# Kernel optimization log

Hardware: AMD Instinct MI355X
Metric: run time of the kernel (lower is better)

The kernel has to match this reference:

```python
import jax, jax.numpy as jnp
import numpy as np

N_NODES = 50000
N_EDGES = 1600000
NEG_SLOPE = 0.2


def setup_inputs() -> dict:
    key = jax.random.key(0)
    ks = jax.random.split(key, 11)
    s = 0.1  # small init scale
    return {
        "x": jax.random.normal(ks[0], (N_NODES, 128), dtype=jnp.float32),
        "edge_index": jax.random.randint(ks[1], (2, N_EDGES), 0, N_NODES, dtype=jnp.int64),
        "W1": jax.random.normal(ks[2], (128, 128), dtype=jnp.float32) * s,
        "att_src1": jax.random.normal(ks[3], (2, 64), dtype=jnp.float32) * s,
        "att_dst1": jax.random.normal(ks[4], (2, 64), dtype=jnp.float32) * s,
        "b1": jax.random.normal(ks[5], (128,), dtype=jnp.float32) * s,
        "W2": jax.random.normal(ks[6], (128, 64), dtype=jnp.float32) * s,
        "att_src2": jax.random.normal(ks[7], (1, 64), dtype=jnp.float32) * s,
        "att_dst2": jax.random.normal(ks[8], (1, 64), dtype=jnp.float32) * s,
        "b2": jax.random.normal(ks[9], (64,), dtype=jnp.float32) * s,
    }


def gat_conv(x, W, a_src, a_dst, bias, src, dst, n_nodes):
    # x: [N, F_in]; W: [F_in, H*C]; a_src/a_dst: [H, C]; bias: [H*C]
    H, C = a_src.shape
    xl = (x @ W).reshape(n_nodes, H, C)                 # [N,H,C]
    alpha_s = jnp.einsum('nhc,hc->nh', xl, a_src)       # [N,H]
    alpha_d = jnp.einsum('nhc,hc->nh', xl, a_dst)       # [N,H]
    e = jax.nn.leaky_relu(alpha_s[src] + alpha_d[dst], NEG_SLOPE)  # [E,H]
    # segment softmax over edges sharing the same destination node
    m = jax.ops.segment_max(e, dst, num_segments=n_nodes)          # [N,H]
    m = jnp.where(jnp.isfinite(m), m, 0.0)
    e = jnp.exp(e - m[dst])
    denom = jax.ops.segment_sum(e, dst, num_segments=n_nodes)      # [N,H]
    alpha = e / denom[dst]                               # self-loops guarantee denom > 0
    msg = xl[src] * alpha[:, :, None]                    # [E,H,C]
    out = jax.ops.segment_sum(msg, dst, num_segments=n_nodes)      # [N,H,C]
    return out.reshape(n_nodes, H * C) + bias


def reference(x, edge_index, W1, att_src1, att_dst1, b1, W2, att_src2, att_dst2, b2):
    n = x.shape[0]
    # PyG GATConv default add_self_loops=True
    loops = jnp.arange(n, dtype=edge_index.dtype)
    src = jnp.concatenate([edge_index[0], loops])
    dst = jnp.concatenate([edge_index[1], loops])

    h = gat_conv(x, W1, att_src1, att_dst1, b1, src, dst, n)   # [N, 128]
    h = jax.nn.relu(h)                                          # dropout p=0 (eval)
    h = gat_conv(h, W2, att_src2, att_dst2, b2, src, dst, n)   # [N, 64]
    h = jax.nn.relu(h)
    return h
```

## Files before the change

kernel.cpp:

```cpp
#include <hip/hip_runtime.h>
#include <cstdint>
#include <cstddef>

#define NEG_SLOPE 0.2f

#define NB 128
#define LOG_NB 7
#define MAXK 512

__device__ inline unsigned short f2bf(float f) {
    unsigned int u = __float_as_uint(f);
    u += 0x7FFFu + ((u >> 16) & 1u);
    return (unsigned short)(u >> 16);
}
__device__ inline float bf_lo(unsigned int u) { return __uint_as_float(u << 16); }
__device__ inline float bf_hi(unsigned int u) { return __uint_as_float(u & 0xFFFF0000u); }
__device__ inline float bfu(unsigned short u) { return __uint_as_float((unsigned int)u << 16); }

__global__ __launch_bounds__(256) void sort_count_kernel(const int* __restrict__ ei, int E,
                                                         int K, int CH, int* __restrict__ bcnt) {
    __shared__ int hist[4 * MAXK];
    int tid = threadIdx.x;
    int wiw = tid >> 6;
    for (int i = tid; i < K; i += 256) {
        hist[i] = 0; hist[MAXK + i] = 0; hist[2 * MAXK + i] = 0; hist[3 * MAXK + i] = 0;
    }
    __syncthreads();
    int lo = blockIdx.x * CH;
    int hi = lo + CH; if (hi > E) hi = E;
    for (int e = lo + tid; e < hi; e += 256)
        atomicAdd(&hist[wiw * MAXK + (ei[(size_t)E + e] >> LOG_NB)], 1);
    __syncthreads();
    for (int i = tid; i < K; i += 256) {
        int c = hist[i] + hist[MAXK + i] + hist[2 * MAXK + i] + hist[3 * MAXK + i];
        if (c) atomicAdd(&bcnt[i], c);
    }
}

__global__ void sort_scan_kernel(const int* __restrict__ bcnt, int* __restrict__ boff,
                                 int* __restrict__ bcur, int K, int E) {
    __shared__ int buf[MAXK];
    int tid = threadIdx.x;
    int v = (tid < K) ? bcnt[tid] : 0;
    buf[tid] = v;
    __syncthreads();
    for (int o = 1; o < MAXK; o <<= 1) {
        int t = (tid >= o) ? buf[tid - o] : 0;
        __syncthreads();
        buf[tid] += t;
        __syncthreads();
    }
    if (tid < K) {
        int ex = buf[tid] - v;
        boff[tid] = ex;
        bcur[tid] = ex;
    }
    if (tid == K) boff[K] = E;
}


template <int FOUT, int H, int ROWS, bool BF16IN>
__device__ __forceinline__ void gemm_att_body(const void* __restrict__ Xv,
                                              const float* __restrict__ W,
                                              const float* __restrict__ attS,
                                              const float* __restrict__ attD,
                                              unsigned short* __restrict__ Ybf,
                                              float* __restrict__ as_,
                                              float* __restrict__ ad_, int N, int bid,
                                              float* sX, float* sW) {
    constexpr int CG  = FOUT / 4;
    constexpr int RR  = (ROWS * FOUT) / 1024;
    constexpr int LDX = 36;
    int tid = threadIdx.x;
    int rowbase = bid * ROWS;
    int cg = tid % CG;
    int rg = tid / CG;
    int r0 = rg * RR;

    float acc[RR][4];
#pragma unroll
    for (int i = 0; i < RR; i++)
#pragma unroll
        for (int c = 0; c < 4; c++) acc[i][c] = 0.f;

    for (int k0 = 0; k0 < 128; k0 += 32) {
        __syncthreads();
        for (int idx = tid; idx < ROWS * 8; idx += 256) {
            int r = idx >> 3, q = idx & 7;
            int row = rowbase + r;
            float4 val;
            if (row < N) {
                if constexpr (BF16IN) {
                    const unsigned short* Xb = (const unsigned short*)Xv;
                    ushort4 raw = *(const ushort4*)&Xb[(size_t)row * 128 + k0 + q * 4];
                    val = make_float4(bfu(raw.x), bfu(raw.y), bfu(raw.z), bfu(raw.w));
                } else {
                    const float* X = (const float*)Xv;
                    val = *(const float4*)&X[(size_t)row * 128 + k0 + q * 4];
                }
            } else {
                val = make_float4(0.f, 0.f, 0.f, 0.f);
            }
            *(float4*)&sX[r * LDX + q * 4] = val;
        }
        for (int idx = tid; idx < 8 * FOUT; idx += 256)
            *(float4*)&sW[idx * 4] = *(const float4*)&W[(size_t)k0 * FOUT + idx * 4];
        __syncthreads();
        for (int k = 0; k < 32; k += 4) {
            float4 xr[RR];
#pragma unroll
            for (int i = 0; i < RR; i++)
                xr[i] = *(const float4*)&sX[(r0 + i) * LDX + k];
#pragma unroll
            for (int kk = 0; kk < 4; kk++) {
                float4 wv = ((const float4*)(sW + (size_t)(k + kk) * FOUT))[cg];
#pragma unroll
                for (int i = 0; i < RR; i++) {
                    float xv = (&xr[i].x)[kk];
                    acc[i][0] = fmaf(xv, wv.x, acc[i][0]);
                    acc[i][1] = fmaf(xv, wv.y, acc[i][1]);
                    acc[i][2] = fmaf(xv, wv.z, acc[i][2]);
                    acc[i][3] = fmaf(xv, wv.w, acc[i][3]);
                }
            }
        }
    }

#pragma unroll
    for (int i = 0; i < RR; i++) {
        int row = rowbase + r0 + i;
        if (row < N) {
            ushort4 v;
            v.x = f2bf(acc[i][0]); v.y = f2bf(acc[i][1]);
            v.z = f2bf(acc[i][2]); v.w = f2bf(acc[i][3]);
            *(ushort4*)(Ybf + (size_t)row * FOUT + cg * 4) = v;
        }
    }

    float4 asv = ((const float4*)attS)[cg];
    float4 adv = ((const float4*)attD)[cg];
    int head = (H == 2) ? (cg >> 4) : 0;
#pragma unroll
    for (int i = 0; i < RR; i++) {
        float ps = acc[i][0] * asv.x + acc[i][1] * asv.y + acc[i][2] * asv.z + acc[i][3] * asv.w;
        float pd = acc[i][0] * adv.x + acc[i][1] * adv.y + acc[i][2] * adv.z + acc[i][3] * adv.w;
#pragma unroll
        for (int o = 1; o <= 8; o <<= 1) { ps += __shfl_xor(ps, o); pd += __shfl_xor(pd, o); }
        int row = rowbase + r0 + i;
        if ((tid & 15) == 0 && row < N) {
            as_[(size_t)row * H + head] = ps;
            ad_[(size_t)row * H + head] = pd;
        }
    }
}

__global__ __launch_bounds__(256) void scatter_gemm1_kernel(const int* __restrict__ ei, int E,
                                                            int K, int CH, int* __restrict__ bcur,
                                                            unsigned int* __restrict__ bkt,
                                                            const float* __restrict__ X,
                                                            const float* __restrict__ W1,
                                                            const float* __restrict__ attS,
                                                            const float* __restrict__ attD,
                                                            unsigned short* __restrict__ Ybf,
                                                            float* __restrict__ as_,
                                                            float* __restrict__ ad_, int N, int G) {
    __shared__ float sX[64 * 36];
    __shared__ float sW[32 * 128];
    if (blockIdx.x < G) {
        int* hist = (int*)sX;
        int* base = (int*)sW;
        int* cur2 = (int*)sW + MAXK;
        int tid = threadIdx.x;
        int wiw = tid >> 6;
        for (int i = tid; i < K; i += 256) {
            hist[i] = 0; hist[MAXK + i] = 0; hist[2 * MAXK + i] = 0; hist[3 * MAXK + i] = 0;
        }
        __syncthreads();
        int lo = blockIdx.x * CH;
        int hi = lo + CH; if (hi > E) hi = E;
        for (int e = lo + tid; e < hi; e += 256)
            atomicAdd(&hist[wiw * MAXK + (ei[(size_t)E + e] >> LOG_NB)], 1);
        __syncthreads();
        for (int i = tid; i < K; i += 256) {
            int c = hist[i] + hist[MAXK + i] + hist[2 * MAXK + i] + hist[3 * MAXK + i];
            base[i] = c ? atomicAdd(&bcur[i], c) : 0;
            cur2[i] = 0;
        }
        __syncthreads();
        for (int e = lo + tid; e < hi; e += 256) {
            int s = ei[e];
            int d = ei[(size_t)E + e];
            int k = d >> LOG_NB;
            int r = atomicAdd(&cur2[k], 1);
            bkt[(size_t)base[k] + r] = (unsigned int)s | ((unsigned int)d << 16);
        }
    } else {
        gemm_att_body<128, 2, 64, false>(X, W1, attS, attD, Ybf, as_, ad_, N, blockIdx.x - G, sX, sW);
    }
}

__global__ __launch_bounds__(256) void gemm2_kernel(const unsigned short* __restrict__ X,
                                                    const float* __restrict__ W,
                                                    const float* __restrict__ attS,
                                                    const float* __restrict__ attD,
                                                    unsigned short* __restrict__ Ybf,
                                                    float* __restrict__ as_,
                                                    float* __restrict__ ad_, int N) {
    __shared__ float sX[64 * 36];
    __shared__ float sW[32 * 64];
    gemm_att_body<64, 1, 64, true>(X, W, attS, attD, Ybf, as_, ad_, N, blockIdx.x, sX, sW);
}

__global__ __launch_bounds__(256) void sort_finalize_kernel(const unsigned int* __restrict__ bkt,
                                                            const int* __restrict__ boff,
                                                            int* __restrict__ off,
                                                            unsigned int* __restrict__ csrc, int N) {
    __shared__ int nhist[4 * NB];
    __shared__ int part[256];
    __shared__ int loff[NB];
    int k = blockIdx.x;
    int tid = threadIdx.x;
    int wiw = tid >> 6;
    int node0 = k << LOG_NB;
    int nh = N - node0; if (nh > NB) nh = NB;
    int beg = boff[k], end = boff[k + 1];
    for (int i = tid; i < NB; i += 256) {
        nhist[i] = 0; nhist[NB + i] = 0; nhist[2 * NB + i] = 0; nhist[3 * NB + i] = 0;
    }
    __syncthreads();
    for (int e = beg + tid; e < end; e += 256)
        atomicAdd(&nhist[wiw * NB + ((bkt[e] >> 16) - node0)], 1);
    __syncthreads();
    int i0 = 2 * tid, i1 = 2 * tid + 1;
    int v0 = (i0 < nh) ? nhist[i0] + nhist[NB + i0] + nhist[2 * NB + i0] + nhist[3 * NB + i0] + 1 : 0;
    int v1 = (i1 < nh) ? nhist[i1] + nhist[NB + i1] + nhist[2 * NB + i1] + nhist[3 * NB + i1] + 1 : 0;
    part[tid] = v0 + v1;
    __syncthreads();
    for (int o = 1; o < 256; o <<= 1) {
        int t = (tid >= o) ? part[tid - o] : 0;
        __syncthreads();
        part[tid] += t;
        __syncthreads();
    }
    int gbase = beg + node0;
    int base = gbase + ((tid > 0) ? part[tid - 1] : 0);
    if (i0 < nh) loff[i0] = base;
    if (i1 < nh) loff[i1] = base + v0;
    __syncthreads();
    for (int i = tid; i < nh; i += 256) {
        int node = node0 + i;
        off[node] = loff[i];
        csrc[loff[i]] = (unsigned int)node | ((unsigned int)node << 16);
        nhist[i] = loff[i] + 1;
    }
    if (node0 + nh == N && tid == 0) off[N] = gbase + part[255];
    __syncthreads();
    for (int e = beg + tid; e < end; e += 256) {
        unsigned int p = bkt[e];
        int pos = atomicAdd(&nhist[(p >> 16) - node0], 1);
        csrc[pos] = p;
    }
}


__global__ __launch_bounds__(256) void agg1_kernel(const unsigned short* __restrict__ xl,
                                                   const float* __restrict__ as_,
                                                   const float* __restrict__ ad_,
                                                   const float* __restrict__ bias,
                                                   const int* __restrict__ off,
                                                   const unsigned int* __restrict__ csrc,
                                                   unsigned short* __restrict__ out, int N) {
    __shared__ float4 sps[4][64];
    int wiw  = threadIdx.x >> 6;
    int lane = threadIdx.x & 63;
    int node = blockIdx.x * 4 + wiw;
    if (node >= N) return;
    int beg = off[node], end = off[node + 1];
    int deg = end - beg;
    float2 adn = ((const float2*)ad_)[node];

    int cl  = lane & 15;
    int sub = lane >> 4;
    int hd1 = (cl >> 3) & 1;
    float acc[8];
#pragma unroll
    for (int i = 0; i < 8; i++) acc[i] = 0.f;
    const char* xbase = (const char*)xl + cl * 16;

    if (deg <= 64) {
        int so = 0;
        float t0 = -1e30f, t1 = -1e30f;
        if (lane < deg) {
            int s = (int)(csrc[beg + lane] & 0xFFFFu);
            so = s << 8;
            float2 asv = ((const float2*)as_)[s];
            t0 = asv.x + adn.x; t0 = t0 > 0.f ? t0 : NEG_SLOPE * t0;
            t1 = asv.y + adn.y; t1 = t1 > 0.f ? t1 : NEG_SLOPE * t1;
        }
        float m0 = t0, m1 = t1;
#pragma unroll
        for (int o = 32; o; o >>= 1) {
            m0 = fmaxf(m0, __shfl_xor(m0, o));
            m1 = fmaxf(m1, __shfl_xor(m1, o));
        }
        float e0 = (lane < deg) ? __expf(t0 - m0) : 0.f;
        float e1 = (lane < deg) ? __expf(t1 - m1) : 0.f;
        float s0 = e0, s1 = e1;
#pragma unroll
        for (int o = 32; o; o >>= 1) { s0 += __shfl_xor(s0, o); s1 += __shfl_xor(s1, o); }
        sps[wiw][lane] = make_float4(e0 / s0, e1 / s1, __int_as_float(so), 0.f);
        int iters = (deg + 3) >> 2;
#pragma unroll 8
        for (int j = 0; j < iters; j++) {
            float4 q = sps[wiw][j * 4 + sub];
            float a  = hd1 ? q.y : q.x;
            uint4 v  = *(const uint4*)(xbase + __float_as_int(q.z));
            acc[0] = fmaf(a, bf_lo(v.x), acc[0]); acc[1] = fmaf(a, bf_hi(v.x), acc[1]);
            acc[2] = fmaf(a, bf_lo(v.y), acc[2]); acc[3] = fmaf(a, bf_hi(v.y), acc[3]);
            acc[4] = fmaf(a, bf_lo(v.z), acc[4]); acc[5] = fmaf(a, bf_hi(v.z), acc[5]);
            acc[6] = fmaf(a, bf_lo(v.w), acc[6]); acc[7] = fmaf(a, bf_hi(v.w), acc[7]);
        }
    } else {
        float m0 = -1e30f, m1 = -1e30f;
        for (int b = beg; b < end; b += 64) {
            int e = b + lane;
            if (e < end) {
                int s = (int)(csrc[e] & 0xFFFFu);
                float2 asv = ((const float2*)as_)[s];
                float t0 = asv.x + adn.x; t0 = t0 > 0.f ? t0 : NEG_SLOPE * t0;
                float t1 = asv.y + adn.y; t1 = t1 > 0.f ? t1 : NEG_SLOPE * t1;
                m0 = fmaxf(m0, t0); m1 = fmaxf(m1, t1);
            }
        }
#pragma unroll
        for (int o = 32; o; o >>= 1) {
            m0 = fmaxf(m0, __shfl_xor(m0, o));
            m1 = fmaxf(m1, __shfl_xor(m1, o));
        }
        float s0 = 0.f, s1 = 0.f;
        for (int b = beg; b < end; b += 64) {
            int e = b + lane;
            if (e < end) {
                int s = (int)(csrc[e] & 0xFFFFu);
                float2 asv = ((const float2*)as_)[s];
                float t0 = asv.x + adn.x; t0 = t0 > 0.f ? t0 : NEG_SLOPE * t0;
                float t1 = asv.y + adn.y; t1 = t1 > 0.f ? t1 : NEG_SLOPE * t1;
                s0 += __expf(t0 - m0); s1 += __expf(t1 - m1);
            }
        }
#pragma unroll
        for (int o = 32; o; o >>= 1) { s0 += __shfl_xor(s0, o); s1 += __shfl_xor(s1, o); }
        float i0 = 1.f / s0, i1 = 1.f / s1;
        for (int b = beg; b < end; b += 64) {
            int cnt = end - b; if (cnt > 64) cnt = 64;
            float p0 = 0.f, p1 = 0.f; int so = 0;
            if (lane < cnt) {
                int s = (int)(csrc[b + lane] & 0xFFFFu);
                so = s << 8;
                float2 asv = ((const float2*)as_)[s];
                float t0 = asv.x + adn.x; t0 = t0 > 0.f ? t0 : NEG_SLOPE * t0;
                float t1 = asv.y + adn.y; t1 = t1 > 0.f ? t1 : NEG_SLOPE * t1;
                p0 = __expf(t0 - m0) * i0; p1 = __expf(t1 - m1) * i1;
            }
            sps[wiw][lane] = make_float4(p0, p1, __int_as_float(so), 0.f);
            int iters = (cnt + 3) >> 2;
#pragma unroll 8
            for (int j = 0; j < iters; j++) {
                float4 q = sps[wiw][j * 4 + sub];
                float a  = hd1 ? q.y : q.x;
                uint4 v  = *(const uint4*)(xbase + __float_as_int(q.z));
                acc[0] = fmaf(a, bf_lo(v.x), acc[0]); acc[1] = fmaf(a, bf_hi(v.x), acc[1]);
                acc[2] = fmaf(a, bf_lo(v.y), acc[2]); acc[3] = fmaf(a, bf_hi(v.y), acc[3]);
                acc[4] = fmaf(a, bf_lo(v.z), acc[4]); acc[5] = fmaf(a, bf_hi(v.z), acc[5]);
                acc[6] = fmaf(a, bf_lo(v.w), acc[6]); acc[7] = fmaf(a, bf_hi(v.w), acc[7]);
            }
        }
    }
#pragma unroll
    for (int o = 16; o <= 32; o <<= 1)
#pragma unroll
        for (int i = 0; i < 8; i++) acc[i] += __shfl_xor(acc[i], o);
    if (sub == 0) {
        const float* bp = bias + cl * 8;
        unsigned int w0 = (unsigned int)f2bf(fmaxf(acc[0] + bp[0], 0.f)) |
                          ((unsigned int)f2bf(fmaxf(acc[1] + bp[1], 0.f)) << 16);
        unsigned int w1 = (unsigned int)f2bf(fmaxf(acc[2] + bp[2], 0.f)) |
                          ((unsigned int)f2bf(fmaxf(acc[3] + bp[3], 0.f)) << 16);
        unsigned int w2 = (unsigned int)f2bf(fmaxf(acc[4] + bp[4], 0.f)) |
                          ((unsigned int)f2bf(fmaxf(acc[5] + bp[5], 0.f)) << 16);
        unsigned int w3 = (unsigned int)f2bf(fmaxf(acc[6] + bp[6], 0.f)) |
                          ((unsigned int)f2bf(fmaxf(acc[7] + bp[7], 0.f)) << 16);
        uint4 pack = make_uint4(w0, w1, w2, w3);
        *(uint4*)(out + (size_t)node * 128 + cl * 8) = pack;
    }
}


__global__ __launch_bounds__(256) void agg2_kernel(const unsigned short* __restrict__ xl,
                                                   const float* __restrict__ as_,
                                                   const float* __restrict__ ad_,
                                                   const float* __restrict__ bias,
                                                   const int* __restrict__ off,
                                                   const unsigned int* __restrict__ csrc,
                                                   float* __restrict__ out, int N) {
    __shared__ float2 sps[4][64];
    int wiw  = threadIdx.x >> 6;
    int lane = threadIdx.x & 63;
    int node = blockIdx.x * 4 + wiw;
    if (node >= N) return;
    int beg = off[node], end = off[node + 1];
    int deg = end - beg;
    float adn = ad_[node];

    int cl  = lane & 7;
    int sub = lane >> 3;
    float acc[8];
#pragma unroll
    for (int i = 0; i < 8; i++) acc[i] = 0.f;
    const char* xbase = (const char*)xl + cl * 16;

    if (deg <= 64) {
        int so = 0;
        float t = -1e30f;
        if (lane < deg) {
            int s = (int)(csrc[beg + lane] & 0xFFFFu);
            so = s << 7;
            t = as_[s] + adn;
            t = t > 0.f ? t : NEG_SLOPE * t;
        }
        float m = t;
#pragma unroll
        for (int o = 32; o; o >>= 1) m = fmaxf(m, __shfl_xor(m, o));
        float evv = (lane < deg) ? __expf(t - m) : 0.f;
        float sum = evv;
#pragma unroll
        for (int o = 32; o; o >>= 1) sum += __shfl_xor(sum, o);
        sps[wiw][lane] = make_float2(evv / sum, __int_as_float(so));
        int iters = (deg + 7) >> 3;
#pragma unroll 8
        for (int j = 0; j < iters; j++) {
            float2 q = sps[wiw][j * 8 + sub];
            float a  = q.x;
            uint4 v  = *(const uint4*)(xbase + __float_as_int(q.y));
            acc[0] = fmaf(a, bf_lo(v.x), acc[0]); acc[1] = fmaf(a, bf_hi(v.x), acc[1]);
            acc[2] = fmaf(a, bf_lo(v.y), acc[2]); acc[3] = fmaf(a, bf_hi(v.y), acc[3]);
            acc[4] = fmaf(a, bf_lo(v.z), acc[4]); acc[5] = fmaf(a, bf_hi(v.z), acc[5]);
            acc[6] = fmaf(a, bf_lo(v.w), acc[6]); acc[7] = fmaf(a, bf_hi(v.w), acc[7]);
        }
    } else {
        float m = -1e30f;
        for (int b = beg; b < end; b += 64) {
            int e = b + lane;
            if (e < end) {
                float t = as_[csrc[e] & 0xFFFFu] + adn;
                t = t > 0.f ? t : NEG_SLOPE * t;
                m = fmaxf(m, t);
            }
        }
#pragma unroll
        for (int o = 32; o; o >>= 1) m = fmaxf(m, __shfl_xor(m, o));
        float sum = 0.f;
        for (int b = beg; b < end; b += 64) {
            int e = b + lane;
            if (e < end) {
                float t = as_[csrc[e] & 0xFFFFu] + adn;
                t = t > 0.f ? t : NEG_SLOPE * t;
                sum += __expf(t - m);
            }
        }
#pragma unroll
        for (int o = 32; o; o >>= 1) sum += __shfl_xor(sum, o);
        float inv = 1.f / sum;
        for (int b = beg; b < end; b += 64) {
            int cnt = end - b; if (cnt > 64) cnt = 64;
            float p = 0.f; int so = 0;
            if (lane < cnt) {
                int s = (int)(csrc[b + lane] & 0xFFFFu);
                so = s << 7;
                float t = as_[s] + adn;
                t = t > 0.f ? t : NEG_SLOPE * t;
                p = __expf(t - m) * inv;
            }
            sps[wiw][lane] = make_float2(p, __int_as_float(so));
            int iters = (cnt + 7) >> 3;
#pragma unroll 8
            for (int j = 0; j < iters; j++) {
                float2 q = sps[wiw][j * 8 + sub];
                float a  = q.x;
                uint4 v  = *(const uint4*)(xbase + __float_as_int(q.y));
                acc[0] = fmaf(a, bf_lo(v.x), acc[0]); acc[1] = fmaf(a, bf_hi(v.x), acc[1]);
                acc[2] = fmaf(a, bf_lo(v.y), acc[2]); acc[3] = fmaf(a, bf_hi(v.y), acc[3]);
                acc[4] = fmaf(a, bf_lo(v.z), acc[4]); acc[5] = fmaf(a, bf_hi(v.z), acc[5]);
                acc[6] = fmaf(a, bf_lo(v.w), acc[6]); acc[7] = fmaf(a, bf_hi(v.w), acc[7]);
            }
        }
    }
#pragma unroll
    for (int o = 8; o <= 32; o <<= 1)
#pragma unroll
        for (int i = 0; i < 8; i++) acc[i] += __shfl_xor(acc[i], o);
    if (sub == 0) {
        float* op = out + (size_t)node * 64 + cl * 8;
        const float* bp = bias + cl * 8;
#pragma unroll
        for (int i = 0; i < 8; i++) op[i] = fmaxf(acc[i] + bp[i], 0.f);
    }
}


extern "C" void kernel_launch(void* const* d_in, const int* in_sizes, int n_in,
                              void* d_out, int out_size, void* d_ws, size_t ws_size,
                              hipStream_t stream) {
    const float* x        = (const float*)d_in[0];
    const int*   ei       = (const int*)d_in[1];
    const float* W1       = (const float*)d_in[2];
    const float* attS1    = (const float*)d_in[3];
    const float* attD1    = (const float*)d_in[4];
    const float* b1       = (const float*)d_in[5];
    const float* W2       = (const float*)d_in[6];
    const float* attS2    = (const float*)d_in[7];
    const float* attD2    = (const float*)d_in[8];
    const float* b2       = (const float*)d_in[9];
    float* out            = (float*)d_out;

    int N  = in_sizes[0] / 128;
    int E  = in_sizes[1] / 2;
    int EE = E + N;
    int K  = (N + NB - 1) >> LOG_NB;

    char* w = (char*)d_ws;
    auto alloc = [&](size_t bytes) -> void* {
        void* p = (void*)w;
        w += (bytes + 255) & ~(size_t)255;
        return p;
    };
    int*   bcnt = (int*)alloc((size_t)(K + 1) * 4);
    int*   boff = (int*)alloc((size_t)(K + 1) * 4);
    int*   bcur = (int*)alloc((size_t)(K + 1) * 4);
    int*   off  = (int*)alloc((size_t)(N + 1) * 4);
    unsigned int* csrc = (unsigned int*)alloc((size_t)EE * 4);
    unsigned int* bkt  = (unsigned int*)alloc((size_t)E * 4);
    unsigned short* xl1 = (unsigned short*)alloc((size_t)N * 128 * 2);
    float* sd1  = (float*)alloc((size_t)N * 2 * 4);
    float* dd1  = (float*)alloc((size_t)N * 2 * 4);
    unsigned short* h1 = (unsigned short*)alloc((size_t)N * 128 * 2);

    unsigned short* xl2 = xl1;
    float* sd2 = sd1;
    float* dd2 = dd1;

    hipMemsetAsync(bcnt, 0, (size_t)(K + 1) * 4, stream);

    int G   = 256;
    int CH  = (E + G - 1) / G;
    int GB1 = (N + 63) / 64;
    sort_count_kernel<<<G, 256, 0, stream>>>(ei, E, K, CH, bcnt);
    sort_scan_kernel<<<1, MAXK, 0, stream>>>(bcnt, boff, bcur, K, E);
    scatter_gemm1_kernel<<<G + GB1, 256, 0, stream>>>(ei, E, K, CH, bcur, bkt,
                                                      x, W1, attS1, attD1, xl1, sd1, dd1, N, G);
    sort_finalize_kernel<<<K, 256, 0, stream>>>(bkt, boff, off, csrc, N);

    agg1_kernel<<<(N + 3) / 4, 256, 0, stream>>>(xl1, sd1, dd1, b1, off, csrc, h1, N);

    gemm2_kernel<<<(N + 63) / 64, 256, 0, stream>>>(h1, W2, attS2, attD2, xl2, sd2, dd2, N);
    agg2_kernel<<<(N + 3) / 4, 256, 0, stream>>>(xl2, sd2, dd2, b2, off, csrc, out, N);
}
```

Measured before the change: 298.8 us.

## Split layer-1 aggregation into alpha pass and feature-chunked gather over chunked xl layout

Layer-1 GEMM now writes its bf16 output in four column chunks of 32 features (chunk-major, 64 bytes per node per chunk). A separate alpha1 kernel computes the per-edge softmax weights once and stores them as fp16 packed with the source index. A chunked aggregation kernel then gathers one chunk at a time, with blocks for different chunks interleaved. The aim is a smaller per-chunk working set (about 3.2 MB) that stays cache-resident during the random gathers. The cost is an extra kernel launch, an extra write and read of two per-edge arrays, and fp16 precision on the attention weights.

```diff
diff --git a/kernel.cpp b/kernel.cpp
--- a/kernel.cpp
+++ b/kernel.cpp
@@ -1,4 +1,5 @@
 #include <hip/hip_runtime.h>
+#include <hip/hip_fp16.h>
 #include <cstdint>
 #include <cstddef>
 
@@ -16,6 +17,7 @@
 __device__ inline float bf_lo(unsigned int u) { return __uint_as_float(u << 16); }
 __device__ inline float bf_hi(unsigned int u) { return __uint_as_float(u & 0xFFFF0000u); }
 __device__ inline float bfu(unsigned short u) { return __uint_as_float((unsigned int)u << 16); }
+__device__ inline float lrelu(float t) { return t > 0.f ? t : NEG_SLOPE * t; }
 
 __global__ __launch_bounds__(256) void sort_count_kernel(const int* __restrict__ ei, int E,
                                                          int K, int CH, int* __restrict__ bcnt) {
@@ -59,7 +61,7 @@
 }
 
 
-template <int FOUT, int H, int ROWS, bool BF16IN>
+template <int FOUT, int H, int ROWS, bool BF16IN, bool CHUNK_OUT>
 __device__ __forceinline__ void gemm_att_body(const void* __restrict__ Xv,
                                               const float* __restrict__ W,
                                               const float* __restrict__ attS,
@@ -133,7 +135,13 @@
             ushort4 v;
             v.x = f2bf(acc[i][0]); v.y = f2bf(acc[i][1]);
             v.z = f2bf(acc[i][2]); v.w = f2bf(acc[i][3]);
-            *(ushort4*)(Ybf + (size_t)row * FOUT + cg * 4) = v;
+            if constexpr (CHUNK_OUT) {
+                int chunk = cg >> 3;
+                int wc = (cg & 7) * 4;
+                *(ushort4*)(Ybf + ((size_t)chunk * N + row) * 32 + wc) = v;
+            } else {
+                *(ushort4*)(Ybf + (size_t)row * FOUT + cg * 4) = v;
+            }
         }
     }
 
@@ -195,7 +203,8 @@
             bkt[(size_t)base[k] + r] = (unsigned int)s | ((unsigned int)d << 16);
         }
     } else {
-        gemm_att_body<128, 2, 64, false>(X, W1, attS, attD, Ybf, as_, ad_, N, blockIdx.x - G, sX, sW);
+        gemm_att_body<128, 2, 64, false, true>(X, W1, attS, attD, Ybf, as_, ad_, N,
+                                               blockIdx.x - G, sX, sW);
     }
 }
 
@@ -208,7 +217,7 @@
                                                     float* __restrict__ ad_, int N) {
     __shared__ float sX[64 * 36];
     __shared__ float sW[32 * 64];
-    gemm_att_body<64, 1, 64, true>(X, W, attS, attD, Ybf, as_, ad_, N, blockIdx.x, sX, sW);
+    gemm_att_body<64, 1, 64, true, false>(X, W, attS, attD, Ybf, as_, ad_, N, blockIdx.x, sX, sW);
 }
 
 __global__ __launch_bounds__(256) void sort_finalize_kernel(const unsigned int* __restrict__ bkt,
@@ -263,14 +272,12 @@
 }
 
 
-__global__ __launch_bounds__(256) void agg1_kernel(const unsigned short* __restrict__ xl,
-                                                   const float* __restrict__ as_,
-                                                   const float* __restrict__ ad_,
-                                                   const float* __restrict__ bias,
-                                                   const int* __restrict__ off,
-                                                   const unsigned int* __restrict__ csrc,
-                                                   unsigned short* __restrict__ out, int N) {
-    __shared__ float4 sps[4][64];
+__global__ __launch_bounds__(256) void alpha1_kernel(const float* __restrict__ as_,
+                                                     const float* __restrict__ ad_,
+                                                     const int* __restrict__ off,
+                                                     const unsigned int* __restrict__ csrc,
+                                                     unsigned int* __restrict__ pae0,
+                                                     unsigned int* __restrict__ pae1, int N) {
     int wiw  = threadIdx.x >> 6;
     int lane = threadIdx.x & 63;
     int node = blockIdx.x * 4 + wiw;
@@ -278,24 +285,16 @@
     int beg = off[node], end = off[node + 1];
     int deg = end - beg;
     float2 adn = ((const float2*)ad_)[node];
-
-    int cl  = lane & 15;
-    int sub = lane >> 4;
-    int hd1 = (cl >> 3) & 1;
-    float acc[8];
-#pragma unroll
-    for (int i = 0; i < 8; i++) acc[i] = 0.f;
-    const char* xbase = (const char*)xl + cl * 16;
+    (void)wiw;
 
     if (deg <= 64) {
-        int so = 0;
+        int s = 0;
         float t0 = -1e30f, t1 = -1e30f;
         if (lane < deg) {
-            int s = (int)(csrc[beg + lane] & 0xFFFFu);
-            so = s << 8;
+            s = (int)(csrc[beg + lane] & 0xFFFFu);
             float2 asv = ((const float2*)as_)[s];
-            t0 = asv.x + adn.x; t0 = t0 > 0.f ? t0 : NEG_SLOPE * t0;
-            t1 = asv.y + adn.y; t1 = t1 > 0.f ? t1 : NEG_SLOPE * t1;
+            t0 = lrelu(asv.x + adn.x);
+            t1 = lrelu(asv.y + adn.y);
         }
         float m0 = t0, m1 = t1;
 #pragma unroll
@@ -308,17 +307,11 @@
         float s0 = e0, s1 = e1;
 #pragma unroll
         for (int o = 32; o; o >>= 1) { s0 += __shfl_xor(s0, o); s1 += __shfl_xor(s1, o); }
-        sps[wiw][lane] = make_float4(e0 / s0, e1 / s1, __int_as_float(so), 0.f);
-        int iters = (deg + 3) >> 2;
-#pragma unroll 8
-        for (int j = 0; j < iters; j++) {
-            float4 q = sps[wiw][j * 4 + sub];
-            float a  = hd1 ? q.y : q.x;
-            uint4 v  = *(const uint4*)(xbase + __float_as_int(q.z));
-            acc[0] = fmaf(a, bf_lo(v.x), acc[0]); acc[1] = fmaf(a, bf_hi(v.x), acc[1]);
-            acc[2] = fmaf(a, bf_lo(v.y), acc[2]); acc[3] = fmaf(a, bf_hi(v.y), acc[3]);
-            acc[4] = fmaf(a, bf_lo(v.z), acc[4]); acc[5] = fmaf(a, bf_hi(v.z), acc[5]);
-            acc[6] = fmaf(a, bf_lo(v.w), acc[6]); acc[7] = fmaf(a, bf_hi(v.w), acc[7]);
+        if (lane < deg) {
+            unsigned int h0 = (unsigned int)__half_as_ushort(__float2half(e0 / s0));
+            unsigned int h1 = (unsigned int)__half_as_ushort(__float2half(e1 / s1));
+            pae0[beg + lane] = (unsigned int)s | (h0 << 16);
+            pae1[beg + lane] = (unsigned int)s | (h1 << 16);
         }
     } else {
         float m0 = -1e30f, m1 = -1e30f;
@@ -327,9 +320,8 @@
             if (e < end) {
                 int s = (int)(csrc[e] & 0xFFFFu);
                 float2 asv = ((const float2*)as_)[s];
-                float t0 = asv.x + adn.x; t0 = t0 > 0.f ? t0 : NEG_SLOPE * t0;
-                float t1 = asv.y + adn.y; t1 = t1 > 0.f ? t1 : NEG_SLOPE * t1;
-                m0 = fmaxf(m0, t0); m1 = fmaxf(m1, t1);
+                m0 = fmaxf(m0, lrelu(asv.x + adn.x));
+                m1 = fmaxf(m1, lrelu(asv.y + adn.y));
             }
         }
 #pragma unroll
@@ -343,45 +335,79 @@
             if (e < end) {
                 int s = (int)(csrc[e] & 0xFFFFu);
                 float2 asv = ((const float2*)as_)[s];
-                float t0 = asv.x + adn.x; t0 = t0 > 0.f ? t0 : NEG_SLOPE * t0;
-                float t1 = asv.y + adn.y; t1 = t1 > 0.f ? t1 : NEG_SLOPE * t1;
-                s0 += __expf(t0 - m0); s1 += __expf(t1 - m1);
+                s0 += __expf(lrelu(asv.x + adn.x) - m0);
+                s1 += __expf(lrelu(asv.y + adn.y) - m1);
             }
         }
 #pragma unroll
         for (int o = 32; o; o >>= 1) { s0 += __shfl_xor(s0, o); s1 += __shfl_xor(s1, o); }
         float i0 = 1.f / s0, i1 = 1.f / s1;
         for (int b = beg; b < end; b += 64) {
-            int cnt = end - b; if (cnt > 64) cnt = 64;
-            float p0 = 0.f, p1 = 0.f; int so = 0;
-            if (lane < cnt) {
-                int s = (int)(csrc[b + lane] & 0xFFFFu);
-                so = s << 8;
+            int e = b + lane;
+            if (e < end) {
+                int s = (int)(csrc[e] & 0xFFFFu);
                 float2 asv = ((const float2*)as_)[s];
-                float t0 = asv.x + adn.x; t0 = t0 > 0.f ? t0 : NEG_SLOPE * t0;
-                float t1 = asv.y + adn.y; t1 = t1 > 0.f ? t1 : NEG_SLOPE * t1;
-                p0 = __expf(t0 - m0) * i0; p1 = __expf(t1 - m1) * i1;
-            }
-            sps[wiw][lane] = make_float4(p0, p1, __int_as_float(so), 0.f);
-            int iters = (cnt + 3) >> 2;
-#pragma unroll 8
-            for (int j = 0; j < iters; j++) {
-                float4 q = sps[wiw][j * 4 + sub];
-                float a  = hd1 ? q.y : q.x;
-                uint4 v  = *(const uint4*)(xbase + __float_as_int(q.z));
-                acc[0] = fmaf(a, bf_lo(v.x), acc[0]); acc[1] = fmaf(a, bf_hi(v.x), acc[1]);
-                acc[2] = fmaf(a, bf_lo(v.y), acc[2]); acc[3] = fmaf(a, bf_hi(v.y), acc[3]);
-                acc[4] = fmaf(a, bf_lo(v.z), acc[4]); acc[5] = fmaf(a, bf_hi(v.z), acc[5]);
-                acc[6] = fmaf(a, bf_lo(v.w), acc[6]); acc[7] = fmaf(a, bf_hi(v.w), acc[7]);
-            }
-        }
-    }
-#pragma unroll
-    for (int o = 16; o <= 32; o <<= 1)
+                float a0 = __expf(lrelu(asv.x + adn.x) - m0) * i0;
+                float a1 = __expf(lrelu(asv.y + adn.y) - m1) * i1;
+                unsigned int h0 = (unsigned int)__half_as_ushort(__float2half(a0));
+                unsigned int h1 = (unsigned int)__half_as_ushort(__float2half(a1));
+                pae0[e] = (unsigned int)s | (h0 << 16);
+                pae1[e] = (unsigned int)s | (h1 << 16);
+            }
+        }
+    }
+}
+
+
+__global__ __launch_bounds__(256) void chunk_agg1_kernel(const unsigned short* __restrict__ xlc,
+                                                         const unsigned int* __restrict__ pae0,
+                                                         const unsigned int* __restrict__ pae1,
+                                                         const float* __restrict__ bias,
+                                                         const int* __restrict__ off,
+                                                         unsigned short* __restrict__ out,
+                                                         int N) {
+    int bid   = blockIdx.x;
+    int slot  = bid & 7;
+    int chunk = slot & 3;
+    int half  = slot >> 2;
+    int blkin = (bid >> 3) * 2 + half;
+    int wiw   = threadIdx.x >> 6;
+    int lane  = threadIdx.x & 63;
+    int node  = blkin * 4 + wiw;
+    if (node >= N) return;
+
+    int beg = off[node];
+    int deg = off[node + 1] - beg;
+    int le = lane >> 2;
+    int li = lane & 3;
+
+    const unsigned int* pae = (chunk & 2) ? pae1 : pae0;
+    const char* xb = (const char*)xlc + ((size_t)chunk * N) * 64 + li * 16;
+
+    float acc[8];
+#pragma unroll
+    for (int i = 0; i < 8; i++) acc[i] = 0.f;
+
+    int rounds = (deg + 15) >> 4;
+#pragma unroll 4
+    for (int r = 0; r < rounds; r++) {
+        int e = r * 16 + le;
+        unsigned int p = (e < deg) ? pae[beg + e] : 0u;
+        float a = __half2float(__ushort_as_half((unsigned short)(p >> 16)));
+        int s = (int)(p & 0xFFFFu);
+        uint4 v = *(const uint4*)(xb + ((size_t)s << 6));
+        acc[0] = fmaf(a, bf_lo(v.x), acc[0]); acc[1] = fmaf(a, bf_hi(v.x), acc[1]);
+        acc[2] = fmaf(a, bf_lo(v.y), acc[2]); acc[3] = fmaf(a, bf_hi(v.y), acc[3]);
+        acc[4] = fmaf(a, bf_lo(v.z), acc[4]); acc[5] = fmaf(a, bf_hi(v.z), acc[5]);
+        acc[6] = fmaf(a, bf_lo(v.w), acc[6]); acc[7] = fmaf(a, bf_hi(v.w), acc[7]);
+    }
+#pragma unroll
+    for (int o = 4; o <= 32; o <<= 1)
 #pragma unroll
         for (int i = 0; i < 8; i++) acc[i] += __shfl_xor(acc[i], o);
-    if (sub == 0) {
-        const float* bp = bias + cl * 8;
+
+    if (lane < 4) {
+        const float* bp = bias + chunk * 32 + lane * 8;
         unsigned int w0 = (unsigned int)f2bf(fmaxf(acc[0] + bp[0], 0.f)) |
                           ((unsigned int)f2bf(fmaxf(acc[1] + bp[1], 0.f)) << 16);
         unsigned int w1 = (unsigned int)f2bf(fmaxf(acc[2] + bp[2], 0.f)) |
@@ -390,8 +416,7 @@
                           ((unsigned int)f2bf(fmaxf(acc[5] + bp[5], 0.f)) << 16);
         unsigned int w3 = (unsigned int)f2bf(fmaxf(acc[6] + bp[6], 0.f)) |
                           ((unsigned int)f2bf(fmaxf(acc[7] + bp[7], 0.f)) << 16);
-        uint4 pack = make_uint4(w0, w1, w2, w3);
-        *(uint4*)(out + (size_t)node * 128 + cl * 8) = pack;
+        *(uint4*)(out + (size_t)node * 128 + chunk * 32 + lane * 8) = make_uint4(w0, w1, w2, w3);
     }
 }
 
@@ -544,6 +569,8 @@
     float* sd1  = (float*)alloc((size_t)N * 2 * 4);
     float* dd1  = (float*)alloc((size_t)N * 2 * 4);
     unsigned short* h1 = (unsigned short*)alloc((size_t)N * 128 * 2);
+    unsigned int* pae0 = (unsigned int*)alloc((size_t)EE * 4);
+    unsigned int* pae1 = (unsigned int*)alloc((size_t)EE * 4);
 
     unsigned short* xl2 = xl1;
     float* sd2 = sd1;
@@ -560,7 +587,9 @@
                                                       x, W1, attS1, attD1, xl1, sd1, dd1, N, G);
     sort_finalize_kernel<<<K, 256, 0, stream>>>(bkt, boff, off, csrc, N);
 
-    agg1_kernel<<<(N + 3) / 4, 256, 0, stream>>>(xl1, sd1, dd1, b1, off, csrc, h1, N);
+    alpha1_kernel<<<(N + 3) / 4, 256, 0, stream>>>(sd1, dd1, off, csrc, pae0, pae1, N);
+    int CAB = ((N + 7) / 8) * 8;
+    chunk_agg1_kernel<<<CAB, 256, 0, stream>>>(xl1, pae0, pae1, b1, off, h1, N);
 
     gemm2_kernel<<<(N + 63) / 64, 256, 0, stream>>>(h1, W2, attS2, attD2, xl2, sd2, dd2, N);
     agg2_kernel<<<(N + 3) / 4, 256, 0, stream>>>(xl2, sd2, dd2, b2, off, csrc, out, N);
```

After: 339.3 us. 1.14x slower.
